# Optimization experiments

Hardware: AMD Instinct MI355X
Metric: run time of the kernel (lower is better)

Reference implementation:

```python
import jax, jax.numpy as jnp
import numpy as np

B, S, D, E, N = 2, 1024, 1024, 64, 16  # batch, seq, model_dim, embedding_dim, num_splats


def setup_inputs() -> dict:
    key = jax.random.key(0)
    ks = jax.random.split(key, 8)
    inv_sqrt_d = 1.0 / np.sqrt(D)
    return {
        "token_embeddings": jax.random.normal(ks[0], (B, S, D), jnp.float32),
        # position encoder Linear(D, E)
        "pos_W": jax.random.normal(ks[1], (D, E), jnp.float32) * inv_sqrt_d,
        "pos_b": jnp.zeros((E,), jnp.float32),
        "positional_bias": jax.random.normal(ks[2], (1024, E), jnp.float32) * 0.01,
        "splat_positions": jax.random.normal(ks[3], (N, E), jnp.float32) * 0.2,
        "splat_log_scales": jnp.zeros((N,), jnp.float32),
        # q/k/v Linear(D, D, bias=False)
        "q_W": jax.random.normal(ks[4], (D, D), jnp.float32) * inv_sqrt_d,
        "k_W": jax.random.normal(ks[5], (D, D), jnp.float32) * inv_sqrt_d,
        "v_W": jax.random.normal(ks[6], (D, D), jnp.float32) * inv_sqrt_d,
        "splat_gates": jnp.full((N,), 0.5, jnp.float32),
        "residual_weight": jnp.asarray(0.8, jnp.float32),
        "ln_w": jnp.ones((D,), jnp.float32),
        "ln_b": jnp.zeros((D,), jnp.float32),
    }


def reference(token_embeddings, pos_W, pos_b, positional_bias, splat_positions,
              splat_log_scales, q_W, k_W, v_W, splat_gates, residual_weight,
              ln_w, ln_b):
    b, s, d = token_embeddings.shape
    # token positions in splat embedding space: tanh(Linear(x)) + pos_bias[:S]
    positions = jnp.tanh(token_embeddings @ pos_W + pos_b) + positional_bias[:s][None]  # [B,S,E]
    # spatial influence per splat: Gaussian of distance, clamped scales, floor 0.01
    diff = positions[:, :, None, :] - splat_positions[None, None]  # [B,S,N,E]
    dist_sq = jnp.sum(diff * diff, axis=-1)                         # [B,S,N]
    scales = jnp.clip(jnp.exp(splat_log_scales), 0.3, 2.0)
    influence = jnp.maximum(jnp.exp(-0.5 * dist_sq / (scales * scales)), 0.01)  # [B,S,N]

    q = token_embeddings @ q_W
    k = token_embeddings @ k_W
    v = token_embeddings @ v_W

    w = jnp.transpose(influence, (2, 0, 1))      # [N,B,S]
    qw = q[None] * w[..., None]                  # [N,B,S,D]
    kw = k[None] * w[..., None]
    scores = jnp.einsum('nbid,nbjd->nbij', qw, kw) / jnp.sqrt(jnp.asarray(d, jnp.float32))
    causal = jnp.tril(jnp.ones((s, s), bool))
    scores = jnp.where(causal[None, None], scores, -1e9)
    attn = jax.nn.softmax(scores, axis=-1)       # [N,B,S,S]
    out = jnp.einsum('nbij,bjd->nbid', attn, v)  # [N,B,S,D]

    gates = jax.nn.sigmoid(splat_gates)[:, None, None, None]
    combined = jnp.mean(out * gates, axis=0)     # [B,S,D]

    rw = jax.nn.sigmoid(residual_weight)
    o = rw * token_embeddings + (1.0 - rw) * combined
    # LayerNorm (eps=1e-5)
    mu = jnp.mean(o, axis=-1, keepdims=True)
    var = jnp.mean((o - mu) ** 2, axis=-1, keepdims=True)
    return (o - mu) / jnp.sqrt(var + 1e-5) * ln_w + ln_b
```

## Files before the change

kernel.cpp:

```cpp
#include <hip/hip_runtime.h>
#include <hip/hip_bf16.h>
#include <hip/hip_fp16.h>

using bf16 = __hip_bfloat16;
typedef __attribute__((ext_vector_type(8))) short short8;
typedef __attribute__((ext_vector_type(4))) float f32x4;

static constexpr int Bb = 2, Ss = 1024, Dd = 1024, Ee = 64, Nn = 16;

struct Params {
    const float *X, *posW, *posB, *pbias, *spos, *lsc, *qW, *kW, *vW, *gates, *rwp, *lnw, *lnb;
    bf16 *Xb, *Wt, *WpT, *QKV, *Vt, *Aav;
    __half *wh;
    float *qk, *cb, *out;
};

__device__ __forceinline__ unsigned short f2bfr(float f) {
    __hip_bfloat16 h = __float2bfloat16(f);
    return *reinterpret_cast<unsigned short*>(&h);
}

#define GL_LDS(gp, lp) __builtin_amdgcn_global_load_lds( \
    (const __attribute__((address_space(1))) void*)(gp), \
    (__attribute__((address_space(3))) void*)(lp), 16, 0, 0)

__device__ __forceinline__ void do_transpose_f2b(
    const float* __restrict__ in, bf16* __restrict__ out,
    int R, int C, int bx, int by, char* sm)
{
    float (*tile)[65] = (float(*)[65])sm;
    int tx = threadIdx.x & 63, ty = threadIdx.x >> 6;
    int r0 = by * 64, c0 = bx * 64;
    #pragma unroll
    for (int i = 0; i < 16; ++i)
        tile[ty + i*4][tx] = in[(long)(r0 + ty + i*4)*C + c0 + tx];
    __syncthreads();
    #pragma unroll
    for (int i = 0; i < 16; ++i)
        out[(long)(c0 + ty + i*4)*R + r0 + tx] = __float2bfloat16(tile[tx][ty + i*4]);
    __syncthreads();
}

__device__ __forceinline__ void do_gemm6464(
    const bf16* __restrict__ Ab, const bf16* __restrict__ Bw, float* __restrict__ C,
    int Nc, int m0, int n0, int kBeg, int kEnd, float scale, char* sm)
{
    int tid = threadIdx.x, wid = tid >> 6, lane = tid & 63;
    int r16 = lane & 15, quad = lane >> 4;

    f32x4 acc[4];
    #pragma unroll
    for (int j = 0; j < 4; ++j)
        #pragma unroll
        for (int c = 0; c < 4; ++c) acc[j][c] = 0.f;

    const short* Ag = (const short*)Ab;
    const short* Bg = (const short*)Bw;

    int row2[2], kg2[2];
    #pragma unroll
    for (int j = 0; j < 2; ++j) {
        int c = tid + j*256; row2[j] = c >> 3; kg2[j] = (c & 7) ^ (row2[j] & 7);
    }

    auto stage = [&](int k0, int cr) {
        short* sA = (short*)(sm + cr*16384);
        short* sB = (short*)(sm + cr*16384 + 8192);
        #pragma unroll
        for (int j = 0; j < 2; ++j) {
            GL_LDS(Ag + (long)(m0 + row2[j])*1024 + k0 + kg2[j]*8, sA + (tid + j*256)*8);
            GL_LDS(Bg + (long)(n0 + row2[j])*1024 + k0 + kg2[j]*8, sB + (tid + j*256)*8);
        }
    };

    stage(kBeg, 0);
    __syncthreads();
    int cur = 0;
    for (int k0 = kBeg; k0 < kEnd; k0 += 64) {
        if (k0 + 64 < kEnd) stage(k0 + 64, cur ^ 1);
        short* lA = (short*)(sm + cur*16384);
        short* lB = (short*)(sm + cur*16384 + 8192);
        #pragma unroll
        for (int kk = 0; kk < 2; ++kk) {
            int kc = kk*4 + quad;
            int ra = wid*16 + r16;
            short8 af = *(const short8*)(lA + ra*64 + (kc ^ (ra & 7))*8);
            #pragma unroll
            for (int j = 0; j < 4; ++j) {
                int rb = j*16 + r16;
                short8 bfv = *(const short8*)(lB + rb*64 + (kc ^ (rb & 7))*8);
                acc[j] = __builtin_amdgcn_mfma_f32_16x16x32_bf16(af, bfv, acc[j], 0, 0, 0);
            }
        }
        __syncthreads();
        cur ^= 1;
    }

    #pragma unroll
    for (int j = 0; j < 4; ++j)
        #pragma unroll
        for (int rr = 0; rr < 4; ++rr)
            C[(long)(m0 + wid*16 + quad*4 + rr)*Nc + n0 + j*16 + r16] =
                acc[j][rr] * scale;
}

template<int OUT>
__device__ __forceinline__ void do_gemm64x128(
    const bf16* __restrict__ Ab, const bf16* __restrict__ Bw, void* __restrict__ Cv,
    int Nc, int m0, int n0, char* sm)
{
    int tid = threadIdx.x, wid = tid >> 6, lane = tid & 63;
    int wn = wid * 32, r16 = lane & 15, quad = lane >> 4;

    f32x4 acc[4][2];
    #pragma unroll
    for (int i = 0; i < 4; ++i)
        #pragma unroll
        for (int j = 0; j < 2; ++j)
            #pragma unroll
            for (int c = 0; c < 4; ++c) acc[i][j][c] = 0.f;

    const short* Ag = (const short*)Ab;
    const short* Bg = (const short*)Bw;

    int arow[2], akg[2], brow[4], bkg[4];
    #pragma unroll
    for (int j = 0; j < 2; ++j) {
        int c = tid + j*256; arow[j] = c >> 3; akg[j] = (c & 7) ^ (arow[j] & 7);
    }
    #pragma unroll
    for (int j = 0; j < 4; ++j) {
        int c = tid + j*256; brow[j] = c >> 3; bkg[j] = (c & 7) ^ (brow[j] & 7);
    }

    auto stage = [&](int k0, int cr) {
        short* sA = (short*)(sm + cr*24576);
        short* sB = (short*)(sm + cr*24576 + 8192);
        #pragma unroll
        for (int j = 0; j < 2; ++j)
            GL_LDS(Ag + (long)(m0 + arow[j])*1024 + k0 + akg[j]*8, sA + (tid + j*256)*8);
        #pragma unroll
        for (int j = 0; j < 4; ++j)
            GL_LDS(Bg + (long)(n0 + brow[j])*1024 + k0 + bkg[j]*8, sB + (tid + j*256)*8);
    };

    stage(0, 0);
    __syncthreads();
    int cur = 0;
    for (int k0 = 0; k0 < 1024; k0 += 64) {
        if (k0 + 64 < 1024) stage(k0 + 64, cur ^ 1);
        short* lA = (short*)(sm + cur*24576);
        short* lB = (short*)(sm + cur*24576 + 8192);
        #pragma unroll
        for (int kk = 0; kk < 2; ++kk) {
            int kc = kk*4 + quad;
            short8 af[4], bfv[2];
            #pragma unroll
            for (int i = 0; i < 4; ++i) {
                int r = i*16 + r16;
                af[i] = *(const short8*)(lA + r*64 + (kc ^ (r & 7))*8);
            }
            #pragma unroll
            for (int j = 0; j < 2; ++j) {
                int r = wn + j*16 + r16;
                bfv[j] = *(const short8*)(lB + r*64 + (kc ^ (r & 7))*8);
            }
            #pragma unroll
            for (int i = 0; i < 4; ++i)
                #pragma unroll
                for (int j = 0; j < 2; ++j)
                    acc[i][j] = __builtin_amdgcn_mfma_f32_16x16x32_bf16(af[i], bfv[j], acc[i][j], 0, 0, 0);
        }
        __syncthreads();
        cur ^= 1;
    }

    if (OUT == 1) {
        ushort (*lt)[136] = (ushort(*)[136])sm;
        #pragma unroll
        for (int i = 0; i < 4; ++i)
            #pragma unroll
            for (int j = 0; j < 2; ++j)
                #pragma unroll
                for (int rr = 0; rr < 4; ++rr)
                    lt[i*16 + quad*4 + rr][wn + j*16 + r16] = f2bfr(acc[i][j][rr]);
        __syncthreads();
        ushort* C = (ushort*)Cv;
        #pragma unroll
        for (int q = 0; q < 4; ++q) {
            int c = tid + q*256;
            int row = c >> 4, off = (c & 15) * 8;
            *(uint4*)(C + (long)(m0 + row)*Nc + n0 + off) = *(const uint4*)&lt[row][off];
        }
    } else {
        ushort (*lt)[72] = (ushort(*)[72])sm;
        #pragma unroll
        for (int i = 0; i < 4; ++i)
            #pragma unroll
            for (int j = 0; j < 2; ++j)
                #pragma unroll
                for (int rr = 0; rr < 4; ++rr)
                    lt[wn + j*16 + r16][i*16 + quad*4 + rr] = f2bfr(acc[i][j][rr]);
        __syncthreads();
        ushort* Vb = (ushort*)Cv + (long)(m0 >> 10) * Dd * Ss;
        int s0 = m0 & (Ss - 1);
        #pragma unroll
        for (int q = 0; q < 4; ++q) {
            int c = tid + q*256;
            int vrow = c >> 3, off = (c & 7) * 8;
            *(uint4*)(Vb + (long)(n0 + vrow)*Ss + s0 + off) = *(const uint4*)&lt[vrow][off];
        }
    }
}

__device__ __forceinline__ void do_pos(const Params& p, int m0, char* sm)
{
    float (*P)[65]  = (float(*)[65])(sm + 16384);
    float (*sp)[65] = (float(*)[65])(sm + 16384 + 64*65*4);

    int tid = threadIdx.x, wid = tid >> 6, lane = tid & 63;
    int r16 = lane & 15, quad = lane >> 4;

    for (int idx = tid; idx < 16*64; idx += 256)
        sp[idx >> 6][idx & 63] = p.spos[idx];

    f32x4 acc[4];
    #pragma unroll
    for (int j = 0; j < 4; ++j)
        #pragma unroll
        for (int c = 0; c < 4; ++c) acc[j][c] = 0.f;

    int ra = tid >> 2, ka = (tid & 3) * 8;
    const short* Ag = (const short*)p.Xb;
    const short* Bg = (const short*)p.WpT;

    auto stage = [&](int k0, int cr) {
        short* sA = (short*)(sm + cr*8192);
        short* sB = (short*)(sm + cr*8192 + 4096);
        GL_LDS(Ag + (long)(m0+ra)*1024 + k0 + ka, sA + tid*8);
        GL_LDS(Bg + (long)ra*1024 + k0 + ka,      sB + tid*8);
    };

    stage(0, 0);
    __syncthreads();
    int cur = 0;
    for (int k0 = 0; k0 < Dd; k0 += 32) {
        if (k0 + 32 < Dd) stage(k0 + 32, cur ^ 1);
        short* lA = (short*)(sm + cur*8192);
        short* lB = (short*)(sm + cur*8192 + 4096);
        short8 af = *(const short8*)(lA + (wid*16 + r16)*32 + quad*8);
        #pragma unroll
        for (int j = 0; j < 4; ++j) {
            short8 bfv = *(const short8*)(lB + (j*16 + r16)*32 + quad*8);
            acc[j] = __builtin_amdgcn_mfma_f32_16x16x32_bf16(af, bfv, acc[j], 0, 0, 0);
        }
        __syncthreads();
        cur ^= 1;
    }

    #pragma unroll
    for (int j = 0; j < 4; ++j)
        #pragma unroll
        for (int rr = 0; rr < 4; ++rr) {
            int rl  = wid*16 + quad*4 + rr;
            int col = j*16 + r16;
            int srow = (m0 + rl) & (Ss - 1);
            P[rl][col] = tanhf(acc[j][rr] + p.posB[col]) + p.pbias[srow*Ee + col];
        }
    __syncthreads();

    int n  = tid & 15;
    int rb = (tid >> 4) * 4;
    float sc = __expf(p.lsc[n]);
    sc = fminf(fmaxf(sc, 0.3f), 2.0f);
    float inv2 = -0.5f / (sc * sc);
    #pragma unroll
    for (int rr = 0; rr < 4; ++rr) {
        int row = rb + rr;
        float d2 = 0.f;
        #pragma unroll 16
        for (int e = 0; e < 64; ++e) {
            float df = P[row][e] - sp[n][e];
            d2 += df * df;
        }
        float infl = fmaxf(__expf(d2 * inv2), 0.01f);
        p.wh[(long)(m0 + row)*Nn + n] = __float2half(infl);
    }
}

__global__ __launch_bounds__(256) void k_prep(Params p)
{
    __shared__ __align__(16) char sm[64*65*4];
    int z = blockIdx.z;
    if (z < 3) {
        const float* w = (z == 0) ? p.qW : (z == 1) ? p.kW : p.vW;
        do_transpose_f2b(w, p.Wt + (long)z*Dd*Dd, Dd, Dd, blockIdx.x, blockIdx.y, sm);
    } else if (blockIdx.x == 0) {
        do_transpose_f2b(p.posW, p.WpT, Dd, Ee, 0, blockIdx.y, sm);
    } else {
        int job = blockIdx.y * 15 + (blockIdx.x - 1);
        const float4* src = (const float4*)p.X;
        ushort4* dst = (ushort4*)p.Xb;
        for (int idx = job*256 + (int)threadIdx.x; idx < Bb*Ss*Dd/4; idx += 240*256) {
            float4 v = src[idx];
            ushort4 y;
            y.x = f2bfr(v.x); y.y = f2bfr(v.y); y.z = f2bfr(v.z); y.w = f2bfr(v.w);
            dst[idx] = y;
        }
    }
}

__global__ __launch_bounds__(256) void k_qkv_pos(Params p)
{
    __shared__ __align__(16) char sm[49152];
    int job = blockIdx.x;
    if (job < 32) {
        do_pos(p, job*64, sm);
    } else {
        int t = job - 32;
        int g = t >> 8;
        int r = t & 255;
        int bm = r >> 3, bn = r & 7;
        if (g < 2)
            do_gemm64x128<1>(p.Xb, p.Wt + (long)g*Dd*Dd, p.QKV + (long)g*2048*1024,
                             Dd, bm*64, bn*128, sm);
        else
            do_gemm64x128<2>(p.Xb, p.Wt + (long)2*Dd*Dd, p.Vt,
                             Dd, bm*64, bn*128, sm);
    }
}

__global__ __launch_bounds__(256) void k_qkt(Params p)
{
    __shared__ __align__(16) char sm[32768];
    int job = blockIdx.x;
    int b = job / 136, t = job % 136;
    int acc = 0, bm = 0, bn = 0;
    #pragma unroll
    for (int u = 0; u < 16; ++u) {
        int c = u + 1;
        if (t < acc + c) { bm = u; bn = t - acc; break; }
        acc += c;
    }
    const bf16* Qb = p.QKV + (long)b*Ss*Dd;
    const bf16* Kb = p.QKV + (long)2048*1024 + (long)b*Ss*Dd;
    float* dst = p.qk + (long)b*Ss*Ss;
    do_gemm6464(Qb, Kb, dst, Ss, bm*64, bn*64, 0, 1024, 0.03125f, sm);
}

__global__ __launch_bounds__(256) void k_softmax(Params p)
{
    __shared__ __align__(16) char sm[36864 + 256 + 16384];
    __half2 (*wt)[9] = (__half2(*)[9])sm;
    float (*wi4)[16] = (float(*)[16])(sm + 36864);
    float (*qc)[Ss]  = (float(*)[Ss])(sm + 36864 + 256);

    int base = blockIdx.x * 4, b = blockIdx.y;
    int tid = threadIdx.x, wid = tid >> 6, lane = tid & 63;
    int imax = base + 3;

    const __half*  whb  = p.wh + (long)b*Ss*Nn;
    const __half2* whb2 = (const __half2*)whb;

    for (int j = tid; j <= imax; j += 256) {
        #pragma unroll
        for (int h = 0; h < 8; ++h)
            wt[j][h] = whb2[j*8 + h];
    }
    if (tid < 64) wi4[tid >> 4][tid & 15] =
        __half2float(whb[(long)(base + (tid >> 4))*16 + (tid & 15)]);
    __syncthreads();

    int i = base + wid;
    long roff = ((long)b*Ss + i)*Ss;
    const float* q0 = p.qk + roff;
    bf16* arow      = p.Aav + roff;

    float wiR[16], l[16];
    #pragma unroll
    for (int n = 0; n < 16; ++n) { wiR[n] = wi4[wid][n]; l[n] = 0.f; }

    for (int j = lane; j <= i; j += 64) {
        float q = q0[j];
        qc[wid][j] = q;
        #pragma unroll
        for (int h = 0; h < 8; ++h) {
            float2 f = __half22float2(wt[j][h]);
            l[2*h]     += __expf(wiR[2*h]     * f.x * q);
            l[2*h + 1] += __expf(wiR[2*h + 1] * f.y * q);
        }
    }
    #pragma unroll
    for (int n = 0; n < 16; ++n)
        #pragma unroll
        for (int off = 32; off > 0; off >>= 1)
            l[n] += __shfl_xor(l[n], off);

    float coef[16];
    #pragma unroll
    for (int n = 0; n < 16; ++n) {
        float g  = p.gates[n];
        float sg = 1.f / (1.f + __expf(-g));
        coef[n]  = sg / (16.f * l[n]);
    }

    int jLim = (i | 63) + 1;
    for (int j = lane; j < jLim; j += 64) {
        float a = 0.f;
        if (j <= i) {
            float q = qc[wid][j];
            #pragma unroll
            for (int h = 0; h < 8; ++h) {
                float2 f = __half22float2(wt[j][h]);
                a += coef[2*h]     * __expf(wiR[2*h]     * f.x * q);
                a += coef[2*h + 1] * __expf(wiR[2*h + 1] * f.y * q);
            }
        }
        arow[j] = __float2bfloat16(a);
    }
}

__global__ __launch_bounds__(256) void k_av(Params p)
{
    __shared__ __align__(16) char sm[32768];
    int job = blockIdx.x;
    int b  = job >> 8;
    int r  = job & 255;
    int bm = 15 - (r >> 4);
    int bn = r & 15;
    int kEnd = (bm + 1) * 64;

    const bf16* Ab = p.Aav + (long)b*Ss*Ss;
    const bf16* Bw = p.Vt + (long)b*Dd*Ss;
    float* dst = p.cb + (long)b*Ss*Dd;
    do_gemm6464(Ab, Bw, dst, Dd, bm*64, bn*64, 0, kEnd, 1.f, sm);
}

__global__ __launch_bounds__(256) void k_epilogue(Params p)
{
    __shared__ float rs[4], rq[4];
    long row = blockIdx.x;
    int tid = threadIdx.x, wid = tid >> 6, lane = tid & 63;
    float rw = 1.f / (1.f + __expf(-p.rwp[0]));

    float4 c  = ((const float4*)(p.cb + row*Dd))[tid];
    float4 xv = ((const float4*)(p.X + row*Dd))[tid];

    float o[4];
    o[0] = rw * xv.x + (1.f - rw) * c.x;
    o[1] = rw * xv.y + (1.f - rw) * c.y;
    o[2] = rw * xv.z + (1.f - rw) * c.z;
    o[3] = rw * xv.w + (1.f - rw) * c.w;

    float sm1 = o[0] + o[1] + o[2] + o[3];
    float sq  = o[0]*o[0] + o[1]*o[1] + o[2]*o[2] + o[3]*o[3];
    #pragma unroll
    for (int off = 32; off > 0; off >>= 1) { sm1 += __shfl_xor(sm1, off); sq += __shfl_xor(sq, off); }
    if (lane == 0) { rs[wid] = sm1; rq[wid] = sq; }
    __syncthreads();
    sm1 = rs[0] + rs[1] + rs[2] + rs[3];
    sq  = rq[0] + rq[1] + rq[2] + rq[3];
    float mu  = sm1 * (1.f/1024.f);
    float var = sq * (1.f/1024.f) - mu*mu;
    float inv = rsqrtf(var + 1e-5f);

    float4 lw = ((const float4*)p.lnw)[tid];
    float4 lb = ((const float4*)p.lnb)[tid];
    float4 y;
    y.x = (o[0] - mu)*inv*lw.x + lb.x;
    y.y = (o[1] - mu)*inv*lw.y + lb.y;
    y.z = (o[2] - mu)*inv*lw.z + lb.z;
    y.w = (o[3] - mu)*inv*lw.w + lb.w;
    ((float4*)(p.out + row*Dd))[tid] = y;
}

extern "C" void kernel_launch(void* const* d_in, const int* in_sizes, int n_in,
                              void* d_out, int out_size, void* d_ws, size_t ws_size,
                              hipStream_t stream)
{
    Params prm;
    prm.X     = (const float*)d_in[0];
    prm.posW  = (const float*)d_in[1];
    prm.posB  = (const float*)d_in[2];
    prm.pbias = (const float*)d_in[3];
    prm.spos  = (const float*)d_in[4];
    prm.lsc   = (const float*)d_in[5];
    prm.qW    = (const float*)d_in[6];
    prm.kW    = (const float*)d_in[7];
    prm.vW    = (const float*)d_in[8];
    prm.gates = (const float*)d_in[9];
    prm.rwp   = (const float*)d_in[10];
    prm.lnw   = (const float*)d_in[11];
    prm.lnb   = (const float*)d_in[12];

    char* ws = (char*)d_ws;
    size_t off = 0;
    prm.Xb  = (bf16*)(ws + off);   off += (size_t)Bb*Ss*Dd*2;
    prm.Wt  = (bf16*)(ws + off);   off += (size_t)3*Dd*Dd*2;
    prm.WpT = (bf16*)(ws + off);   off += (size_t)Ee*Dd*2;
    prm.QKV = (bf16*)(ws + off);   off += (size_t)2*2048*1024*2;
    prm.Vt  = (bf16*)(ws + off);   off += (size_t)Bb*Dd*Ss*2;
    prm.Aav = (bf16*)(ws + off);   off += (size_t)Bb*Ss*Ss*2;
    prm.wh  = (__half*)(ws + off); off += (size_t)Bb*Ss*Nn*2;
    prm.qk  = (float*)(ws + off);  off += (size_t)Bb*Ss*Ss*4;
    prm.cb  = (float*)(ws + off);  off += (size_t)Bb*Ss*Dd*4;
    prm.out = (float*)d_out;
    (void)ws_size;

    k_prep    <<<dim3(16,16,4), 256, 0, stream>>>(prm);
    k_qkv_pos <<<800,            256, 0, stream>>>(prm);
    k_qkt     <<<272,            256, 0, stream>>>(prm);
    k_softmax <<<dim3(256, 2),   256, 0, stream>>>(prm);
    k_av      <<<512,            256, 0, stream>>>(prm);
    k_epilogue<<<2048,           256, 0, stream>>>(prm);
}
```

Measured before the change: 165.1 us.

## Fuse all stages into one persistent kernel with hierarchical grid barriers

The six separate kernel launches are merged into one persistent kernel of 768 blocks. Each block loops over the work items of a stage, and the stages are separated by a two-level atomic grid barrier. The softmax also drops its shared-memory cache of the score row and re-reads it from global memory, which shrinks LDS so three blocks fit per CU. This removes launch gaps and tail idle between stages, but adds barrier cost, relies on all 768 blocks being co-resident, and needs a barrier-counter memset each call.

```diff
diff --git a/kernel.cpp b/kernel.cpp
--- a/kernel.cpp
+++ b/kernel.cpp
@@ -7,12 +7,14 @@
 typedef __attribute__((ext_vector_type(4))) float f32x4;
 
 static constexpr int Bb = 2, Ss = 1024, Dd = 1024, Ee = 64, Nn = 16;
+static constexpr int NBLK = 768;
 
 struct Params {
     const float *X, *posW, *posB, *pbias, *spos, *lsc, *qW, *kW, *vW, *gates, *rwp, *lnw, *lnb;
     bf16 *Xb, *Wt, *WpT, *QKV, *Vt, *Aav;
     __half *wh;
     float *qk, *cb, *out;
+    unsigned *bar;
 };
 
 __device__ __forceinline__ unsigned short f2bfr(float f) {
@@ -24,6 +26,30 @@
     (const __attribute__((address_space(1))) void*)(gp), \
     (__attribute__((address_space(3))) void*)(lp), 16, 0, 0)
 
+__device__ __forceinline__ void gridbar(unsigned* bar)
+{
+    __syncthreads();
+    if (threadIdx.x == 0) {
+        __threadfence();
+        unsigned g = __hip_atomic_load(&bar[544], __ATOMIC_RELAXED, __HIP_MEMORY_SCOPE_AGENT);
+        unsigned* lc = &bar[(blockIdx.x & 31u) * 16u];
+        unsigned mem = gridDim.x >> 5;
+        unsigned lo = __hip_atomic_fetch_add(lc, 1u, __ATOMIC_RELAXED, __HIP_MEMORY_SCOPE_AGENT);
+        if (lo == mem - 1u) {
+            __hip_atomic_store(lc, 0u, __ATOMIC_RELAXED, __HIP_MEMORY_SCOPE_AGENT);
+            unsigned ro = __hip_atomic_fetch_add(&bar[512], 1u, __ATOMIC_RELAXED, __HIP_MEMORY_SCOPE_AGENT);
+            if (ro == 31u) {
+                __hip_atomic_store(&bar[512], 0u, __ATOMIC_RELAXED, __HIP_MEMORY_SCOPE_AGENT);
+                __hip_atomic_store(&bar[544], g + 1u, __ATOMIC_RELEASE, __HIP_MEMORY_SCOPE_AGENT);
+            }
+        }
+        while (__hip_atomic_load(&bar[544], __ATOMIC_RELAXED, __HIP_MEMORY_SCOPE_AGENT) == g)
+            __builtin_amdgcn_s_sleep(2);
+        __threadfence();
+    }
+    __syncthreads();
+}
+
 __device__ __forceinline__ void do_transpose_f2b(
     const float* __restrict__ in, bf16* __restrict__ out,
     int R, int C, int bx, int by, char* sm)
@@ -31,6 +57,7 @@
     float (*tile)[65] = (float(*)[65])sm;
     int tx = threadIdx.x & 63, ty = threadIdx.x >> 6;
     int r0 = by * 64, c0 = bx * 64;
+    __syncthreads();
     #pragma unroll
     for (int i = 0; i < 16; ++i)
         tile[ty + i*4][tx] = in[(long)(r0 + ty + i*4)*C + c0 + tx];
@@ -73,6 +100,7 @@
         }
     };
 
+    __syncthreads();
     stage(kBeg, 0);
     __syncthreads();
     int cur = 0;
@@ -144,6 +172,7 @@
             GL_LDS(Bg + (long)(n0 + brow[j])*1024 + k0 + bkg[j]*8, sB + (tid + j*256)*8);
     };
 
+    __syncthreads();
     stage(0, 0);
     __syncthreads();
     int cur = 0;
@@ -221,6 +250,7 @@
     int tid = threadIdx.x, wid = tid >> 6, lane = tid & 63;
     int r16 = lane & 15, quad = lane >> 4;
 
+    __syncthreads();
     for (int idx = tid; idx < 16*64; idx += 256)
         sp[idx >> 6][idx & 63] = p.spos[idx];
 
@@ -288,80 +318,19 @@
     }
 }
 
-__global__ __launch_bounds__(256) void k_prep(Params p)
-{
-    __shared__ __align__(16) char sm[64*65*4];
-    int z = blockIdx.z;
-    if (z < 3) {
-        const float* w = (z == 0) ? p.qW : (z == 1) ? p.kW : p.vW;
-        do_transpose_f2b(w, p.Wt + (long)z*Dd*Dd, Dd, Dd, blockIdx.x, blockIdx.y, sm);
-    } else if (blockIdx.x == 0) {
-        do_transpose_f2b(p.posW, p.WpT, Dd, Ee, 0, blockIdx.y, sm);
-    } else {
-        int job = blockIdx.y * 15 + (blockIdx.x - 1);
-        const float4* src = (const float4*)p.X;
-        ushort4* dst = (ushort4*)p.Xb;
-        for (int idx = job*256 + (int)threadIdx.x; idx < Bb*Ss*Dd/4; idx += 240*256) {
-            float4 v = src[idx];
-            ushort4 y;
-            y.x = f2bfr(v.x); y.y = f2bfr(v.y); y.z = f2bfr(v.z); y.w = f2bfr(v.w);
-            dst[idx] = y;
-        }
-    }
-}
-
-__global__ __launch_bounds__(256) void k_qkv_pos(Params p)
-{
-    __shared__ __align__(16) char sm[49152];
-    int job = blockIdx.x;
-    if (job < 32) {
-        do_pos(p, job*64, sm);
-    } else {
-        int t = job - 32;
-        int g = t >> 8;
-        int r = t & 255;
-        int bm = r >> 3, bn = r & 7;
-        if (g < 2)
-            do_gemm64x128<1>(p.Xb, p.Wt + (long)g*Dd*Dd, p.QKV + (long)g*2048*1024,
-                             Dd, bm*64, bn*128, sm);
-        else
-            do_gemm64x128<2>(p.Xb, p.Wt + (long)2*Dd*Dd, p.Vt,
-                             Dd, bm*64, bn*128, sm);
-    }
-}
-
-__global__ __launch_bounds__(256) void k_qkt(Params p)
-{
-    __shared__ __align__(16) char sm[32768];
-    int job = blockIdx.x;
-    int b = job / 136, t = job % 136;
-    int acc = 0, bm = 0, bn = 0;
-    #pragma unroll
-    for (int u = 0; u < 16; ++u) {
-        int c = u + 1;
-        if (t < acc + c) { bm = u; bn = t - acc; break; }
-        acc += c;
-    }
-    const bf16* Qb = p.QKV + (long)b*Ss*Dd;
-    const bf16* Kb = p.QKV + (long)2048*1024 + (long)b*Ss*Dd;
-    float* dst = p.qk + (long)b*Ss*Ss;
-    do_gemm6464(Qb, Kb, dst, Ss, bm*64, bn*64, 0, 1024, 0.03125f, sm);
-}
-
-__global__ __launch_bounds__(256) void k_softmax(Params p)
-{
-    __shared__ __align__(16) char sm[36864 + 256 + 16384];
+__device__ __forceinline__ void do_softmax(const Params& p, int jb, char* sm)
+{
     __half2 (*wt)[9] = (__half2(*)[9])sm;
     float (*wi4)[16] = (float(*)[16])(sm + 36864);
-    float (*qc)[Ss]  = (float(*)[Ss])(sm + 36864 + 256);
-
-    int base = blockIdx.x * 4, b = blockIdx.y;
+
+    int base = (jb & 255) * 4, b = jb >> 8;
     int tid = threadIdx.x, wid = tid >> 6, lane = tid & 63;
     int imax = base + 3;
 
     const __half*  whb  = p.wh + (long)b*Ss*Nn;
     const __half2* whb2 = (const __half2*)whb;
 
+    __syncthreads();
     for (int j = tid; j <= imax; j += 256) {
         #pragma unroll
         for (int h = 0; h < 8; ++h)
@@ -382,7 +351,6 @@
 
     for (int j = lane; j <= i; j += 64) {
         float q = q0[j];
-        qc[wid][j] = q;
         #pragma unroll
         for (int h = 0; h < 8; ++h) {
             float2 f = __half22float2(wt[j][h]);
@@ -408,7 +376,7 @@
     for (int j = lane; j < jLim; j += 64) {
         float a = 0.f;
         if (j <= i) {
-            float q = qc[wid][j];
+            float q = q0[j];
             #pragma unroll
             for (int h = 0; h < 8; ++h) {
                 float2 f = __half22float2(wt[j][h]);
@@ -420,29 +388,14 @@
     }
 }
 
-__global__ __launch_bounds__(256) void k_av(Params p)
-{
-    __shared__ __align__(16) char sm[32768];
-    int job = blockIdx.x;
-    int b  = job >> 8;
-    int r  = job & 255;
-    int bm = 15 - (r >> 4);
-    int bn = r & 15;
-    int kEnd = (bm + 1) * 64;
-
-    const bf16* Ab = p.Aav + (long)b*Ss*Ss;
-    const bf16* Bw = p.Vt + (long)b*Dd*Ss;
-    float* dst = p.cb + (long)b*Ss*Dd;
-    do_gemm6464(Ab, Bw, dst, Dd, bm*64, bn*64, 0, kEnd, 1.f, sm);
-}
-
-__global__ __launch_bounds__(256) void k_epilogue(Params p)
-{
-    __shared__ float rs[4], rq[4];
-    long row = blockIdx.x;
+__device__ __forceinline__ void do_epilogue(const Params& p, long row, char* sm)
+{
+    float* rs = (float*)sm;
+    float* rq = rs + 4;
     int tid = threadIdx.x, wid = tid >> 6, lane = tid & 63;
     float rw = 1.f / (1.f + __expf(-p.rwp[0]));
 
+    __syncthreads();
     float4 c  = ((const float4*)(p.cb + row*Dd))[tid];
     float4 xv = ((const float4*)(p.X + row*Dd))[tid];
 
@@ -472,6 +425,86 @@
     y.z = (o[2] - mu)*inv*lw.z + lb.z;
     y.w = (o[3] - mu)*inv*lw.w + lb.w;
     ((float4*)(p.out + row*Dd))[tid] = y;
+}
+
+__global__ __launch_bounds__(256, 3) void k_mega(Params p)
+{
+    __shared__ __align__(16) char sm[49664];
+
+    for (int j = blockIdx.x; j < 1024; j += NBLK) {
+        int x = j & 15, y = (j >> 4) & 15, z = j >> 8;
+        if (z < 3) {
+            const float* w = (z == 0) ? p.qW : (z == 1) ? p.kW : p.vW;
+            do_transpose_f2b(w, p.Wt + (long)z*Dd*Dd, Dd, Dd, x, y, sm);
+        } else if (x == 0) {
+            do_transpose_f2b(p.posW, p.WpT, Dd, Ee, 0, y, sm);
+        } else {
+            int job = y * 15 + (x - 1);
+            const float4* src = (const float4*)p.X;
+            ushort4* dst = (ushort4*)p.Xb;
+            for (int idx = job*256 + (int)threadIdx.x; idx < Bb*Ss*Dd/4; idx += 240*256) {
+                float4 v = src[idx];
+                ushort4 yv;
+                yv.x = f2bfr(v.x); yv.y = f2bfr(v.y); yv.z = f2bfr(v.z); yv.w = f2bfr(v.w);
+                dst[idx] = yv;
+            }
+        }
+    }
+    gridbar(p.bar);
+
+    for (int j = blockIdx.x; j < 800; j += NBLK) {
+        if (j < 32) {
+            do_pos(p, j*64, sm);
+        } else {
+            int t = j - 32;
+            int g = t >> 8;
+            int r = t & 255;
+            int bm = r >> 3, bn = r & 7;
+            if (g < 2)
+                do_gemm64x128<1>(p.Xb, p.Wt + (long)g*Dd*Dd, p.QKV + (long)g*2048*1024,
+                                 Dd, bm*64, bn*128, sm);
+            else
+                do_gemm64x128<2>(p.Xb, p.Wt + (long)2*Dd*Dd, p.Vt,
+                                 Dd, bm*64, bn*128, sm);
+        }
+    }
+    gridbar(p.bar);
+
+    for (int j = blockIdx.x; j < 272; j += NBLK) {
+        int b = j / 136, t = j % 136;
+        int acc = 0, bm = 0, bn = 0;
+        #pragma unroll
+        for (int u = 0; u < 16; ++u) {
+            int c = u + 1;
+            if (t < acc + c) { bm = u; bn = t - acc; break; }
+            acc += c;
+        }
+        const bf16* Qb = p.QKV + (long)b*Ss*Dd;
+        const bf16* Kb = p.QKV + (long)2048*1024 + (long)b*Ss*Dd;
+        float* dst = p.qk + (long)b*Ss*Ss;
+        do_gemm6464(Qb, Kb, dst, Ss, bm*64, bn*64, 0, 1024, 0.03125f, sm);
+    }
+    gridbar(p.bar);
+
+    for (int j = blockIdx.x; j < 512; j += NBLK)
+        do_softmax(p, j, sm);
+    gridbar(p.bar);
+
+    for (int j = blockIdx.x; j < 512; j += NBLK) {
+        int b  = j >> 8;
+        int r  = j & 255;
+        int bm = 15 - (r >> 4);
+        int bn = r & 15;
+        int kEnd = (bm + 1) * 64;
+        const bf16* Ab = p.Aav + (long)b*Ss*Ss;
+        const bf16* Bw = p.Vt + (long)b*Dd*Ss;
+        float* dst = p.cb + (long)b*Ss*Dd;
+        do_gemm6464(Ab, Bw, dst, Dd, bm*64, bn*64, 0, kEnd, 1.f, sm);
+    }
+    gridbar(p.bar);
+
+    for (int j = blockIdx.x; j < 2048; j += NBLK)
+        do_epilogue(p, (long)j, sm);
 }
 
 extern "C" void kernel_launch(void* const* d_in, const int* in_sizes, int n_in,
@@ -504,13 +537,10 @@
     prm.wh  = (__half*)(ws + off); off += (size_t)Bb*Ss*Nn*2;
     prm.qk  = (float*)(ws + off);  off += (size_t)Bb*Ss*Ss*4;
     prm.cb  = (float*)(ws + off);  off += (size_t)Bb*Ss*Dd*4;
+    prm.bar = (unsigned*)(ws + off); off += 4096;
     prm.out = (float*)d_out;
     (void)ws_size;
 
-    k_prep    <<<dim3(16,16,4), 256, 0, stream>>>(prm);
-    k_qkv_pos <<<800,            256, 0, stream>>>(prm);
-    k_qkt     <<<272,            256, 0, stream>>>(prm);
-    k_softmax <<<dim3(256, 2),   256, 0, stream>>>(prm);
-    k_av      <<<512,            256, 0, stream>>>(prm);
-    k_epilogue<<<2048,           256, 0, stream>>>(prm);
-}
+    hipMemsetAsync(prm.bar, 0, 4096, stream);
+    k_mega<<<NBLK, 256, 0, stream>>>(prm);
+}
```

Result: slower. 374.1 us (+126.5%).
